# Performance work log

Measured on AMD Instinct MI355X. Metric: run time of the kernel, lower is better.

Reference implementation:

```python
import jax, jax.numpy as jnp
import numpy as np

INPUT_DIM, HIDDEN_DIM, N_HEADS, N_AGENTS = 256, 512, 8, 64
BATCH, N_ENTITIES = 128, 256


def setup_inputs() -> dict:
    key = jax.random.key(0)
    ks = jax.random.split(key, 6)
    x = jax.random.normal(ks[0], (BATCH, N_ENTITIES, INPUT_DIM), dtype=jnp.float32)
    # encode: LeakyReLU -> Linear(input_dim, hidden_dim)
    W_enc = jax.random.normal(ks[1], (INPUT_DIM, HIDDEN_DIM), dtype=jnp.float32) * (1.0 / np.sqrt(INPUT_DIM))
    b_enc = jnp.zeros((HIDDEN_DIM,), dtype=jnp.float32)
    # per-head full hidden x hidden projections, stacked on head axis
    WQ = jax.random.normal(ks[2], (N_HEADS, HIDDEN_DIM, HIDDEN_DIM), dtype=jnp.float32)
    WK = jax.random.normal(ks[3], (N_HEADS, HIDDEN_DIM, HIDDEN_DIM), dtype=jnp.float32)
    WV = jax.random.normal(ks[4], (N_HEADS, HIDDEN_DIM, HIDDEN_DIM), dtype=jnp.float32)
    return {"x": x, "W_enc": W_enc, "b_enc": b_enc, "WQ": WQ, "WK": WK, "WV": WV, "n_agents": N_AGENTS}


def reference(x, W_enc, b_enc, WQ, WK, WV, n_agents):
    scale = 1.0 / np.sqrt(WQ.shape[-1]).astype(np.float32)
    # encode: LeakyReLU(0.01) then Linear
    h = jax.nn.leaky_relu(x, negative_slope=0.01) @ W_enc + b_enc  # [b, e, H]
    ha = h[:, :n_agents]  # [b, a, H]
    # all heads at once: n = head axis
    Q = jnp.einsum('bah,nhd->nbad', ha, WQ)
    K = jnp.einsum('beh,nhd->nbed', h, WK)
    V = jnp.einsum('beh,nhd->nbed', h, WV)
    scores = jnp.einsum('nbad,nbed->nbae', Q, K) * scale
    p = jax.nn.softmax(scores, axis=-1)
    # redundant renormalization from the original code
    prob = p / (jnp.sum(p, axis=-1, keepdims=True) + 1e-12)
    z = jnp.einsum('nbae,nbed->nbad', prob, V)  # [n, b, a, H]
    return jnp.mean(z, axis=0)  # [b, a, H]
```

## Files before the change

kernel.cpp:

```cpp
#include <hip/hip_runtime.h>
#include <math.h>

#define BATCH  128
#define NENT   256
#define INDIM  256
#define HID    512
#define NHEAD  8
#define NAGENT 64
#define SCALE  0.04419417382415922f


typedef unsigned short u16;
typedef unsigned int   u32;

typedef __bf16 bf16x8  __attribute__((ext_vector_type(8)));
typedef float  floatx4 __attribute__((ext_vector_type(4)));
typedef u32    u32x4   __attribute__((ext_vector_type(4)));
typedef u32    u32x2   __attribute__((ext_vector_type(2)));

union Frag {
    u32x4 s;
    struct { u32x2 lo, hi; } p;
    bf16x8 v;
};

__device__ __forceinline__ u16 f2bf(float x) {
    u32 u = __float_as_uint(x);
    return (u16)((u + 0x7FFFu + ((u >> 16) & 1u)) >> 16);
}
__device__ __forceinline__ float bf2f(u16 b) {
    return __uint_as_float(((u32)b) << 16);
}
__device__ __forceinline__ void split4(const float4& r, ushort4& hh, ushort4& hl) {
    hh.x = f2bf(r.x); hl.x = f2bf(r.x - bf2f(hh.x));
    hh.y = f2bf(r.y); hl.y = f2bf(r.y - bf2f(hh.y));
    hh.z = f2bf(r.z); hl.z = f2bf(r.z - bf2f(hh.z));
    hh.w = f2bf(r.w); hl.w = f2bf(r.w - bf2f(hh.w));
}
__device__ __forceinline__ floatx4 mm(const Frag& a, const Frag& b, floatx4 c) {
    return __builtin_amdgcn_mfma_f32_16x16x32_bf16(a.v, b.v, c, 0, 0, 0);
}
__device__ __forceinline__ void gl16(const u16* g, char* l) {
    __builtin_amdgcn_global_load_lds(
        (const __attribute__((address_space(1))) u32*)g,
        (__attribute__((address_space(3))) u32*)l, 16, 0, 0);
}

__global__ __launch_bounds__(256) void wenc_t_kernel(const float* __restrict__ W,
                                                     u16* __restrict__ Wt_p) {
    __shared__ float tile[64][68];
    const int bid = blockIdx.x;
    const int k0 = (bid & 3) * 64;
    const int d0 = (bid >> 2) * 64;
    const int t = threadIdx.x;
    const int ki = t >> 2, dc = (t & 3) * 16;
    #pragma unroll
    for (int c = 0; c < 4; ++c)
        *(float4*)&tile[ki][dc + c * 4] =
            *(const float4*)(W + (size_t)(k0 + ki) * HID + d0 + dc + c * 4);
    __syncthreads();
    const int dr = t >> 2, kc = (t & 3) * 16;
    #pragma unroll
    for (int c = 0; c < 4; ++c) {
        float4 v = make_float4(tile[kc + c * 4 + 0][dr], tile[kc + c * 4 + 1][dr],
                               tile[kc + c * 4 + 2][dr], tile[kc + c * 4 + 3][dr]);
        ushort4 hh, hl; split4(v, hh, hl);
        const int kk = k0 + kc + c * 4;
        size_t o = (size_t)(d0 + dr) * 512 + (size_t)(kk >> 5) * 64 + (kk & 31);
        *(ushort4*)(Wt_p + o) = hh;
        *(ushort4*)(Wt_p + o + 32) = hl;
    }
}

__global__ __launch_bounds__(256) void enc_kernel(const float* __restrict__ x,
                                                  const u16* __restrict__ Wt_p,
                                                  const float* __restrict__ bias,
                                                  u16* __restrict__ h_p) {
    __shared__ u16 Ah[32][264];
    __shared__ u16 Al[32][264];
    const int r0 = blockIdx.x * 32;
    const int t  = threadIdx.x;
    {
        const int row = t >> 3;
        const float* xr = x + (size_t)(r0 + row) * INDIM;
        #pragma unroll
        for (int j = 0; j < 8; ++j) {
            const int k0 = ((t & 7) + j * 8) * 4;
            float4 v = *(const float4*)(xr + k0);
            v.x = v.x > 0.f ? v.x : 0.01f * v.x;
            v.y = v.y > 0.f ? v.y : 0.01f * v.y;
            v.z = v.z > 0.f ? v.z : 0.01f * v.z;
            v.w = v.w > 0.f ? v.w : 0.01f * v.w;
            ushort4 hh, hl; split4(v, hh, hl);
            *(ushort4*)&Ah[row][k0] = hh;
            *(ushort4*)&Al[row][k0] = hl;
        }
    }
    __syncthreads();

    const int wid = t >> 6, lane = t & 63, l15 = lane & 15, quad = lane >> 4;
    const int mbase = (wid & 1) * 16;
    const int nbase = (wid >> 1) * 256;
    const floatx4 z4 = {0.f, 0.f, 0.f, 0.f};
    floatx4 acc[16];
    #pragma unroll
    for (int i = 0; i < 16; ++i) acc[i] = z4;

    for (int ks = 0; ks < 8; ++ks) {
        const int k = ks * 32 + quad * 8;
        Frag Afh, Afl;
        Afh.s = *(const u32x4*)&Ah[mbase + l15][k];
        Afl.s = *(const u32x4*)&Al[mbase + l15][k];
        #pragma unroll
        for (int nt = 0; nt < 16; ++nt) {
            const int d = nbase + nt * 16 + l15;
            const size_t wo = (size_t)d * 512 + (size_t)ks * 64 + quad * 8;
            Frag Bh, Bl;
            Bh.s = *(const u32x4*)(Wt_p + wo);
            Bl.s = *(const u32x4*)(Wt_p + wo + 32);
            floatx4 c = acc[nt];
            c = __builtin_amdgcn_mfma_f32_16x16x32_bf16(Afh.v, Bh.v, c, 0, 0, 0);
            c = __builtin_amdgcn_mfma_f32_16x16x32_bf16(Afh.v, Bl.v, c, 0, 0, 0);
            c = __builtin_amdgcn_mfma_f32_16x16x32_bf16(Afl.v, Bh.v, c, 0, 0, 0);
            acc[nt] = c;
        }
    }
    #pragma unroll
    for (int nt = 0; nt < 16; ++nt) {
        const int d = nbase + nt * 16 + l15;
        const float bv = bias[d];
        #pragma unroll
        for (int r = 0; r < 4; ++r) {
            const float v = acc[nt][r] + bv;
            const u16 hi = f2bf(v);
            const u16 lo = f2bf(v - bf2f(hi));
            const size_t o = (size_t)(r0 + mbase + quad * 4 + r) * 1024
                           + (size_t)(d >> 5) * 64 + (d & 31);
            h_p[o]      = hi;
            h_p[o + 32] = lo;
        }
    }
}

__global__ __launch_bounds__(256) void ht_kernel(const u16* __restrict__ h_p,
                                                 u16* __restrict__ hT) {
    __shared__ u16 tile[64][72];
    const int bid = blockIdx.x;
    const int dt = bid & 7;
    const int et = (bid >> 3) & 3;
    const int b  = bid >> 5;
    const int t  = threadIdx.x;
    const int r  = t >> 2, cs = (t & 3) * 16;
    const int dg = dt * 64 + cs;
    const u16* src = h_p + (size_t)(b * 256 + et * 64 + r) * 1024
                   + (size_t)(dg >> 5) * 64 + (dg & 31);
    *(ushort4*)&tile[r][cs + 0]  = *(const ushort4*)(src + 0);
    *(ushort4*)&tile[r][cs + 4]  = *(const ushort4*)(src + 4);
    *(ushort4*)&tile[r][cs + 8]  = *(const ushort4*)(src + 8);
    *(ushort4*)&tile[r][cs + 12] = *(const ushort4*)(src + 12);
    __syncthreads();
    const int d = t >> 2, es = (t & 3) * 16;
    u16* dst = hT + (size_t)b * 131072 + (size_t)(dt * 64 + d) * 256 + et * 64 + es;
    #pragma unroll
    for (int c = 0; c < 4; ++c) {
        ushort4 v = make_ushort4(tile[es + c * 4 + 0][d], tile[es + c * 4 + 1][d],
                                 tile[es + c * 4 + 2][d], tile[es + c * 4 + 3][d]);
        *(ushort4*)(dst + c * 4) = v;
    }
}

__global__ __launch_bounds__(256) void wqk_kernel(const float* __restrict__ WQ,
                                                  const float* __restrict__ WK,
                                                  u16* __restrict__ Mt_p) {
    __shared__ u16 Ah[64][72], Al[64][72], Bh[64][72], Bl[64][72];
    const int bid = blockIdx.x;
    const int jt = (bid & 7) * 64;
    const int it = ((bid >> 3) & 7) * 64;
    const int n  = bid >> 6;
    const float* qp = WQ + (size_t)n * 262144;
    const float* kp = WK + (size_t)n * 262144;
    const int t = threadIdx.x;
    const int wid = t >> 6, lane = t & 63, l15 = lane & 15, quad = lane >> 4;
    const int srow = t >> 2, sc = (t & 3) * 16;

    const floatx4 z4 = {0.f, 0.f, 0.f, 0.f};
    floatx4 acc[4];
    #pragma unroll
    for (int i = 0; i < 4; ++i) acc[i] = z4;

    for (int kc = 0; kc < HID; kc += 64) {
        #pragma unroll
        for (int f = 0; f < 4; ++f) {
            float4 va = *(const float4*)(kp + (size_t)(jt + srow) * HID + kc + sc + f * 4);
            ushort4 hh, hl; split4(va, hh, hl);
            *(ushort4*)&Ah[srow][sc + f * 4] = hh;
            *(ushort4*)&Al[srow][sc + f * 4] = hl;
            float4 vb = *(const float4*)(qp + (size_t)(it + srow) * HID + kc + sc + f * 4);
            split4(vb, hh, hl);
            *(ushort4*)&Bh[srow][sc + f * 4] = hh;
            *(ushort4*)&Bl[srow][sc + f * 4] = hl;
        }
        __syncthreads();
        #pragma unroll
        for (int ks = 0; ks < 2; ++ks) {
            const int k = ks * 32 + quad * 8;
            Frag Afh, Afl;
            Afh.s = *(const u32x4*)&Ah[wid * 16 + l15][k];
            Afl.s = *(const u32x4*)&Al[wid * 16 + l15][k];
            #pragma unroll
            for (int nt = 0; nt < 4; ++nt) {
                Frag Bfh, Bfl;
                Bfh.s = *(const u32x4*)&Bh[nt * 16 + l15][k];
                Bfl.s = *(const u32x4*)&Bl[nt * 16 + l15][k];
                floatx4 c = acc[nt];
                c = __builtin_amdgcn_mfma_f32_16x16x32_bf16(Afh.v, Bfh.v, c, 0, 0, 0);
                c = __builtin_amdgcn_mfma_f32_16x16x32_bf16(Afh.v, Bfl.v, c, 0, 0, 0);
                c = __builtin_amdgcn_mfma_f32_16x16x32_bf16(Afl.v, Bfh.v, c, 0, 0, 0);
                acc[nt] = c;
            }
        }
        __syncthreads();
    }
    #pragma unroll
    for (int nt = 0; nt < 4; ++nt)
        #pragma unroll
        for (int r = 0; r < 4; ++r) {
            const float v = acc[nt][r] * SCALE;
            const u16 hi = f2bf(v);
            const u16 lo = f2bf(v - bf2f(hi));
            const int j = jt + wid * 16 + quad * 4 + r;
            const int i = it + nt * 16 + l15;
            const size_t o = (size_t)n * 524288 + (size_t)j * 1024
                           + (size_t)(i >> 5) * 64 + (i & 31);
            Mt_p[o]      = hi;
            Mt_p[o + 32] = lo;
        }
}

__global__ __launch_bounds__(256) void wvt_kernel(const float* __restrict__ WV,
                                                  u16* __restrict__ WVt) {
    __shared__ float tile[64][68];
    const int bid = blockIdx.x;
    const int i0 = (bid & 7) * 64;
    const int o0 = ((bid >> 3) & 7) * 64;
    const int n  = bid >> 6;
    const float* src = WV + (size_t)n * 262144;
    const int t  = threadIdx.x;
    const int di = t >> 2;
    const int dc = (t & 3) * 16;
    #pragma unroll
    for (int c = 0; c < 4; ++c)
        *(float4*)&tile[di][dc + c * 4] =
            *(const float4*)(src + (size_t)(i0 + di) * HID + o0 + dc + c * 4);
    __syncthreads();
    const int dr = t >> 2;
    const int ic = (t & 3) * 16;
    size_t o = (size_t)n * 262144 + (size_t)(o0 + dr) * HID + i0 + ic;
    #pragma unroll
    for (int c = 0; c < 4; ++c) {
        ushort4 v = make_ushort4(f2bf(tile[ic + c * 4 + 0][dr]), f2bf(tile[ic + c * 4 + 1][dr]),
                                 f2bf(tile[ic + c * 4 + 2][dr]), f2bf(tile[ic + c * 4 + 3][dr]));
        *(ushort4*)(WVt + o + c * 4) = v;
    }
}

template<bool USE_HT>
__global__ __launch_bounds__(256, 3) void attn_kernel(const u16* __restrict__ h_p,
                                                      const u16* __restrict__ Mt_p,
                                                      const u16* __restrict__ WVt,
                                                      const u16* __restrict__ hT,
                                                      float* __restrict__ out) {
    constexpr int SMSZ = USE_HT ? 37888 : 53504;
    __shared__ __align__(16) char SM[SMSZ];
    u16*   Th  = (u16*)SM;
    u16*   Tl  = (u16*)(SM + 16640);
    float* S   = (float*)SM;
    float* red = (float*)(SM + (USE_HT ? 36864 : 33792));
    u16*   HbT = (u16*)SM;
    u16*   U   = (u16*)SM;
    u16*   Pt  = (u16*)(SM + (USE_HT ? 0 : 36864));

    const int bid = blockIdx.x;
    const int x7 = bid & 7;
    const int s  = bid >> 3;
    const int at = s & 1;
    const int n  = (x7 >> 1) | (((s >> 1) & 1) << 2);
    const int b  = ((s >> 2) << 1) | (x7 & 1);

    const int tid  = threadIdx.x;
    const int wid  = tid >> 6;
    const int lane = tid & 63;
    const int l15  = lane & 15;
    const int quad = lane >> 4;

    const u16* Mtp = Mt_p + (size_t)n * 524288;
    const u16* Wv  = WVt  + (size_t)n * 262144;
    const u16* hTb = hT + (size_t)b * 131072;
    const size_t hb_base = (size_t)b * 262144;
    const size_t ha_row0 = hb_base + (size_t)(at * 32) * 1024;

    const floatx4 z4 = {0.f, 0.f, 0.f, 0.f};
    floatx4 Sacc[8];
    #pragma unroll
    for (int i = 0; i < 8; ++i) Sacc[i] = z4;

    for (int H = 0; H < 2; ++H) {
        __syncthreads();
        floatx4 Tacc[8];
        #pragma unroll
        for (int i = 0; i < 8; ++i) Tacc[i] = z4;
        const int d0 = H * 256;
        const u16* mtS = (const u16*)SM;
        const u16* haS = (const u16*)(SM + 32768);
        for (int ks = 0; ks < 16; ++ks) {
            #pragma unroll
            for (int j = 0; j < 8; ++j) {
                const int i = wid * 8 + j;
                const int chunk = i >> 2;
                const int row   = (i & 3) * 64 + lane;
                gl16(Mtp + (size_t)(d0 + row) * 1024 + ks * 64 + chunk * 8,
                     SM + i * 1024);
            }
            {
                const int chunk = wid * 2 + (lane >> 5);
                const int row   = lane & 31;
                gl16(h_p + ha_row0 + (size_t)row * 1024 + ks * 64 + chunk * 8,
                     SM + 32768 + wid * 1024);
            }
            __syncthreads();
            Frag Ah0, Al0, Ah1, Al1;
            Ah0.s = *(const u32x4*)(haS + ((quad)     * 32 + l15)      * 8);
            Al0.s = *(const u32x4*)(haS + ((4 + quad) * 32 + l15)      * 8);
            Ah1.s = *(const u32x4*)(haS + ((quad)     * 32 + 16 + l15) * 8);
            Al1.s = *(const u32x4*)(haS + ((4 + quad) * 32 + 16 + l15) * 8);
            #pragma unroll
            for (int nt = 0; nt < 4; ++nt) {
                const int row = (wid * 4 + nt) * 16 + l15;
                Frag Bh, Bl;
                Bh.s = *(const u32x4*)(mtS + ((quad)     * 256 + row) * 8);
                Bl.s = *(const u32x4*)(mtS + ((4 + quad) * 256 + row) * 8);
                floatx4 c0 = Tacc[nt], c1 = Tacc[4 + nt];
                c0 = mm(Ah0, Bh, c0); c0 = mm(Ah0, Bl, c0); c0 = mm(Al0, Bh, c0);
                c1 = mm(Ah1, Bh, c1); c1 = mm(Ah1, Bl, c1); c1 = mm(Al1, Bh, c1);
                Tacc[nt] = c0; Tacc[4 + nt] = c1;
            }
            __syncthreads();
        }
        #pragma unroll
        for (int mt = 0; mt < 2; ++mt)
            #pragma unroll
            for (int nt = 0; nt < 4; ++nt)
                #pragma unroll
                for (int r = 0; r < 4; ++r) {
                    const float v = Tacc[mt * 4 + nt][r];
                    const int a  = mt * 16 + quad * 4 + r;
                    const int dl = (wid * 4 + nt) * 16 + l15;
                    const u16 hi = f2bf(v);
                    Th[a * 260 + dl] = hi;
                    Tl[a * 260 + dl] = f2bf(v - bf2f(hi));
                }
        __syncthreads();
        for (int ks = 0; ks < 8; ++ks) {
            const int kl = ks * 32 + quad * 8;
            const int ko = (H * 8 + ks) * 64 + quad * 8;
            Frag Ahf[4], Alf[4];
            #pragma unroll
            for (int mt = 0; mt < 4; ++mt) {
                const size_t ro = hb_base + (size_t)((wid * 4 + mt) * 16 + l15) * 1024 + ko;
                Ahf[mt].s = *(const u32x4*)(h_p + ro);
                Alf[mt].s = *(const u32x4*)(h_p + ro + 32);
            }
            #pragma unroll
            for (int nt = 0; nt < 2; ++nt) {
                const int ac = nt * 16 + l15;
                Frag Bfh, Bfl;
                Bfh.p.lo = *(const u32x2*)(Th + ac * 260 + kl);
                Bfh.p.hi = *(const u32x2*)(Th + ac * 260 + kl + 4);
                Bfl.p.lo = *(const u32x2*)(Tl + ac * 260 + kl);
                Bfl.p.hi = *(const u32x2*)(Tl + ac * 260 + kl + 4);
                #pragma unroll
                for (int mt = 0; mt < 4; ++mt) {
                    floatx4 c = Sacc[mt * 2 + nt];
                    c = __builtin_amdgcn_mfma_f32_16x16x32_bf16(Ahf[mt].v, Bfh.v, c, 0, 0, 0);
                    c = __builtin_amdgcn_mfma_f32_16x16x32_bf16(Ahf[mt].v, Bfl.v, c, 0, 0, 0);
                    c = __builtin_amdgcn_mfma_f32_16x16x32_bf16(Alf[mt].v, Bfh.v, c, 0, 0, 0);
                    Sacc[mt * 2 + nt] = c;
                }
            }
        }
    }
    __syncthreads();
    #pragma unroll
    for (int mt = 0; mt < 4; ++mt)
        #pragma unroll
        for (int nt = 0; nt < 2; ++nt)
            #pragma unroll
            for (int r = 0; r < 4; ++r) {
                const int e = (wid * 4 + mt) * 16 + quad * 4 + r;
                const int a = nt * 16 + l15;
                S[e * 33 + a] = Sacc[mt * 2 + nt][r];
            }
    __syncthreads();
    {
        const int a   = tid & 31;
        const int seg = tid >> 5;
        float v[32];
        #pragma unroll
        for (int i = 0; i < 32; ++i) v[i] = S[(seg * 32 + i) * 33 + a];
        float mx = v[0];
        #pragma unroll
        for (int i = 1; i < 32; ++i) mx = fmaxf(mx, v[i]);
        red[a * 8 + seg] = mx;
        __syncthreads();
        float gmx = red[a * 8 + 0];
        #pragma unroll
        for (int i = 1; i < 8; ++i) gmx = fmaxf(gmx, red[a * 8 + i]);
        __syncthreads();
        float sum = 0.f;
        #pragma unroll
        for (int i = 0; i < 32; ++i) { v[i] = expf(v[i] - gmx); sum += v[i]; }
        red[a * 8 + seg] = sum;
        __syncthreads();
        float tot = 0.f;
        #pragma unroll
        for (int i = 0; i < 8; ++i) tot += red[a * 8 + i];
        const float inv = 1.0f / tot;
        #pragma unroll
        for (int i = 0; i < 32; ++i)
            Pt[a * 260 + seg * 32 + i] = f2bf(v[i] * inv);
    }
    __syncthreads();
    floatx4 Uacc[16];
    #pragma unroll
    for (int i = 0; i < 16; ++i) Uacc[i] = z4;
    const int d0w = wid * 128;
    if (USE_HT) {
        for (int ep = 0; ep < 4; ++ep) {
            Frag Bc[2][8];
            #pragma unroll
            for (int sb = 0; sb < 2; ++sb)
                #pragma unroll
                for (int dt = 0; dt < 8; ++dt) {
                    const int d = d0w + dt * 16 + l15;
                    Bc[sb][dt].s = *(const u32x4*)(hTb + (size_t)d * 256
                                                   + (2 * ep + sb) * 32 + quad * 8);
                }
            #pragma unroll
            for (int sb = 0; sb < 2; ++sb) {
                const int et = 2 * ep + sb;
                Frag Ap[2];
                #pragma unroll
                for (int mt = 0; mt < 2; ++mt) {
                    const int ar = mt * 16 + l15;
                    Ap[mt].p.lo = *(const u32x2*)(Pt + ar * 260 + et * 32 + quad * 8);
                    Ap[mt].p.hi = *(const u32x2*)(Pt + ar * 260 + et * 32 + quad * 8 + 4);
                }
                #pragma unroll
                for (int dt = 0; dt < 8; ++dt)
                    #pragma unroll
                    for (int mt = 0; mt < 2; ++mt)
                        Uacc[mt * 8 + dt] = __builtin_amdgcn_mfma_f32_16x16x32_bf16(
                            Ap[mt].v, Bc[sb][dt].v, Uacc[mt * 8 + dt], 0, 0, 0);
            }
        }
    } else {
        u32* Hb32 = (u32*)HbT;
        for (int et = 0; et < 8; ++et) {
            {
                const int epi = lane & 15;
                const int q   = lane >> 4;
                const size_t r0p = hb_base + (size_t)(et * 32 + 2 * epi) * 1024;
                #pragma unroll
                for (int c = 0; c < 4; ++c) {
                    const int d0c = d0w + c * 32 + q * 8;
                    const size_t po = (size_t)(d0c >> 5) * 64 + (d0c & 31);
                    u32x4 u0 = *(const u32x4*)(h_p + r0p + po);
                    u32x4 u1 = *(const u32x4*)(h_p + r0p + 1024 + po);
                    #pragma unroll
                    for (int p = 0; p < 4; ++p) {
                        const u32 w0 = (u0[p] & 0xFFFFu) | (u1[p] << 16);
                        const u32 w1 = (u0[p] >> 16) | (u1[p] & 0xFFFF0000u);
                        Hb32[(d0c + 2 * p) * 18 + epi]     = w0;
                        Hb32[(d0c + 2 * p + 1) * 18 + epi] = w1;
                    }
                }
            }
            Frag Ap[2];
            #pragma unroll
            for (int mt = 0; mt < 2; ++mt) {
                const int ar = mt * 16 + l15;
                Ap[mt].p.lo = *(const u32x2*)(Pt + ar * 260 + et * 32 + quad * 8);
                Ap[mt].p.hi = *(const u32x2*)(Pt + ar * 260 + et * 32 + quad * 8 + 4);
            }
            #pragma unroll
            for (int dt = 0; dt < 8; ++dt) {
                const int d = d0w + dt * 16 + l15;
                Frag Bf;
                Bf.p.lo = *(const u32x2*)(HbT + d * 36 + quad * 8);
                Bf.p.hi = *(const u32x2*)(HbT + d * 36 + quad * 8 + 4);
                #pragma unroll
                for (int mt = 0; mt < 2; ++mt)
                    Uacc[mt * 8 + dt] = __builtin_amdgcn_mfma_f32_16x16x32_bf16(
                        Ap[mt].v, Bf.v, Uacc[mt * 8 + dt], 0, 0, 0);
            }
        }
    }
    __syncthreads();
    #pragma unroll
    for (int mt = 0; mt < 2; ++mt)
        #pragma unroll
        for (int dt = 0; dt < 8; ++dt)
            #pragma unroll
            for (int r = 0; r < 4; ++r) {
                const int a = mt * 16 + quad * 4 + r;
                const int d = d0w + dt * 16 + l15;
                U[a * 520 + d] = f2bf(Uacc[mt * 8 + dt][r]);
            }
    __syncthreads();
    floatx4 Zacc[16];
    #pragma unroll
    for (int i = 0; i < 16; ++i) Zacc[i] = z4;
    for (int kp = 0; kp < 8; ++kp) {
        Frag Bw[2][8];
        #pragma unroll
        for (int sb = 0; sb < 2; ++sb) {
            const int k = (kp * 2 + sb) * 32 + quad * 8;
            #pragma unroll
            for (int dt = 0; dt < 8; ++dt) {
                const int dn = (wid * 8 + dt) * 16 + l15;
                Bw[sb][dt].s = *(const u32x4*)(Wv + (size_t)dn * HID + k);
            }
        }
        #pragma unroll
        for (int sb = 0; sb < 2; ++sb) {
            const int k = (kp * 2 + sb) * 32 + quad * 8;
            Frag Au[2];
            #pragma unroll
            for (int mt = 0; mt < 2; ++mt) {
                Au[mt].p.lo = *(const u32x2*)(U + (mt * 16 + l15) * 520 + k);
                Au[mt].p.hi = *(const u32x2*)(U + (mt * 16 + l15) * 520 + k + 4);
            }
            #pragma unroll
            for (int dt = 0; dt < 8; ++dt)
                #pragma unroll
                for (int mt = 0; mt < 2; ++mt)
                    Zacc[mt * 8 + dt] = __builtin_amdgcn_mfma_f32_16x16x32_bf16(
                        Au[mt].v, Bw[sb][dt].v, Zacc[mt * 8 + dt], 0, 0, 0);
        }
    }
    float* ob = out + ((size_t)b * NAGENT + at * 32) * HID;
    #pragma unroll
    for (int mt = 0; mt < 2; ++mt)
        #pragma unroll
        for (int dt = 0; dt < 8; ++dt)
            #pragma unroll
            for (int r = 0; r < 4; ++r) {
                const int a  = mt * 16 + quad * 4 + r;
                const int dn = (wid * 8 + dt) * 16 + l15;
                atomicAdd(ob + (size_t)a * HID + dn, Zacc[mt * 8 + dt][r] * 0.125f);
            }
}

extern "C" void kernel_launch(void* const* d_in, const int* in_sizes, int n_in,
                              void* d_out, int out_size, void* d_ws, size_t ws_size,
                              hipStream_t stream) {
    const float* x     = (const float*)d_in[0];
    const float* W_enc = (const float*)d_in[1];
    const float* b_enc = (const float*)d_in[2];
    const float* WQ    = (const float*)d_in[3];
    const float* WK    = (const float*)d_in[4];
    const float* WV    = (const float*)d_in[5];
    float* out = (float*)d_out;

    char* ws = (char*)d_ws;
    u16* h_p  = (u16*)ws;
    u16* Mt_p = (u16*)(ws + 67108864);
    u16* WVt  = (u16*)(ws + 75497472);
    u16* hT   = (u16*)(ws + 79691776);
    u16* Wt_p = WVt;

    const bool useHT = ws_size >= (size_t)113246208;

    hipMemsetAsync(d_out, 0, (size_t)out_size * sizeof(float), stream);
    wenc_t_kernel<<<32, 256, 0, stream>>>(W_enc, Wt_p);
    enc_kernel<<<1024, 256, 0, stream>>>(x, Wt_p, b_enc, h_p);
    if (useHT) ht_kernel<<<4096, 256, 0, stream>>>(h_p, hT);
    wvt_kernel<<<512, 256, 0, stream>>>(WV, WVt);
    wqk_kernel<<<512, 256, 0, stream>>>(WQ, WK, Mt_p);
    if (useHT)
        attn_kernel<true><<<2048, 256, 0, stream>>>(h_p, Mt_p, WVt, hT, out);
    else
        attn_kernel<false><<<2048, 256, 0, stream>>>(h_p, Mt_p, WVt, hT, out);
}
```

Measured before the change: 894.5 us.

## Stage MFMA B-operands through LDS with direct global-to-LDS loads

Three GEMM phases of the attention kernel now load their global operands with a gl16 global-to-shared primitive into an LDS staging buffer, then read the MFMA fragments from LDS. Before, each lane issued strided 16-byte global loads straight into registers. The goal is coalesced loads and lower register pressure. The cost is extra __syncthreads barriers per k-step, more LDS (USE_HT grows to 51200 bytes), no double buffering, and a remapped output column index in the final projection.

```diff
diff --git a/kernel.cpp b/kernel.cpp
--- a/kernel.cpp
+++ b/kernel.cpp
@@ -270,12 +270,12 @@
                                                       const u16* __restrict__ WVt,
                                                       const u16* __restrict__ hT,
                                                       float* __restrict__ out) {
-    constexpr int SMSZ = USE_HT ? 37888 : 53504;
+    constexpr int SMSZ = USE_HT ? 51200 : 53504;
     __shared__ __align__(16) char SM[SMSZ];
     u16*   Th  = (u16*)SM;
     u16*   Tl  = (u16*)(SM + 16640);
     float* S   = (float*)SM;
-    float* red = (float*)(SM + (USE_HT ? 36864 : 33792));
+    float* red = (float*)(SM + (USE_HT ? 50176 : 33792));
     u16*   HbT = (u16*)SM;
     u16*   U   = (u16*)SM;
     u16*   Pt  = (u16*)(SM + (USE_HT ? 0 : 36864));
@@ -360,32 +360,69 @@
                     Tl[a * 260 + dl] = f2bf(v - bf2f(hi));
                 }
         __syncthreads();
-        for (int ks = 0; ks < 8; ++ks) {
-            const int kl = ks * 32 + quad * 8;
-            const int ko = (H * 8 + ks) * 64 + quad * 8;
-            Frag Ahf[4], Alf[4];
-            #pragma unroll
-            for (int mt = 0; mt < 4; ++mt) {
-                const size_t ro = hb_base + (size_t)((wid * 4 + mt) * 16 + l15) * 1024 + ko;
-                Ahf[mt].s = *(const u32x4*)(h_p + ro);
-                Alf[mt].s = *(const u32x4*)(h_p + ro + 32);
-            }
-            #pragma unroll
-            for (int nt = 0; nt < 2; ++nt) {
-                const int ac = nt * 16 + l15;
-                Frag Bfh, Bfl;
-                Bfh.p.lo = *(const u32x2*)(Th + ac * 260 + kl);
-                Bfh.p.hi = *(const u32x2*)(Th + ac * 260 + kl + 4);
-                Bfl.p.lo = *(const u32x2*)(Tl + ac * 260 + kl);
-                Bfl.p.hi = *(const u32x2*)(Tl + ac * 260 + kl + 4);
+        {
+            const u16* Bs = (const u16*)(SM + 33792);
+            for (int ks = 0; ks < 8; ++ks) {
+                const int ko = (H * 8 + ks) * 64;
+                const int kl = ks * 32 + quad * 8;
                 #pragma unroll
-                for (int mt = 0; mt < 4; ++mt) {
-                    floatx4 c = Sacc[mt * 2 + nt];
-                    c = __builtin_amdgcn_mfma_f32_16x16x32_bf16(Ahf[mt].v, Bfh.v, c, 0, 0, 0);
-                    c = __builtin_amdgcn_mfma_f32_16x16x32_bf16(Ahf[mt].v, Bfl.v, c, 0, 0, 0);
-                    c = __builtin_amdgcn_mfma_f32_16x16x32_bf16(Alf[mt].v, Bfh.v, c, 0, 0, 0);
-                    Sacc[mt * 2 + nt] = c;
+                for (int j = 0; j < 4; ++j) {
+                    const int i = wid * 4 + j;
+                    gl16(h_p + hb_base + (size_t)((i & 3) * 64 + lane) * 1024
+                             + ko + (i >> 2) * 8,
+                         SM + 33792 + i * 1024);
                 }
+                __syncthreads();
+                {
+                    Frag Ahf[4];
+                    #pragma unroll
+                    for (int mt = 0; mt < 4; ++mt)
+                        Ahf[mt].s = *(const u32x4*)(Bs
+                            + ((size_t)quad * 256 + (wid * 4 + mt) * 16 + l15) * 8);
+                    #pragma unroll
+                    for (int nt = 0; nt < 2; ++nt) {
+                        const int ac = nt * 16 + l15;
+                        Frag Bfh, Bfl;
+                        Bfh.p.lo = *(const u32x2*)(Th + ac * 260 + kl);
+                        Bfh.p.hi = *(const u32x2*)(Th + ac * 260 + kl + 4);
+                        Bfl.p.lo = *(const u32x2*)(Tl + ac * 260 + kl);
+                        Bfl.p.hi = *(const u32x2*)(Tl + ac * 260 + kl + 4);
+                        #pragma unroll
+                        for (int mt = 0; mt < 4; ++mt) {
+                            floatx4 c = Sacc[mt * 2 + nt];
+                            c = mm(Ahf[mt], Bfh, c);
+                            c = mm(Ahf[mt], Bfl, c);
+                            Sacc[mt * 2 + nt] = c;
+                        }
+                    }
+                }
+                __syncthreads();
+                #pragma unroll
+                for (int j = 0; j < 4; ++j) {
+                    const int i = wid * 4 + j;
+                    gl16(h_p + hb_base + (size_t)((i & 3) * 64 + lane) * 1024
+                             + ko + 32 + (i >> 2) * 8,
+                         SM + 33792 + i * 1024);
+                }
+                __syncthreads();
+                {
+                    Frag Alf[4];
+                    #pragma unroll
+                    for (int mt = 0; mt < 4; ++mt)
+                        Alf[mt].s = *(const u32x4*)(Bs
+                            + ((size_t)quad * 256 + (wid * 4 + mt) * 16 + l15) * 8);
+                    #pragma unroll
+                    for (int nt = 0; nt < 2; ++nt) {
+                        const int ac = nt * 16 + l15;
+                        Frag Bfh;
+                        Bfh.p.lo = *(const u32x2*)(Th + ac * 260 + kl);
+                        Bfh.p.hi = *(const u32x2*)(Th + ac * 260 + kl + 4);
+                        #pragma unroll
+                        for (int mt = 0; mt < 4; ++mt)
+                            Sacc[mt * 2 + nt] = mm(Alf[mt], Bfh, Sacc[mt * 2 + nt]);
+                    }
+                }
+                __syncthreads();
             }
         }
     }
@@ -435,33 +472,31 @@
     for (int i = 0; i < 16; ++i) Uacc[i] = z4;
     const int d0w = wid * 128;
     if (USE_HT) {
-        for (int ep = 0; ep < 4; ++ep) {
-            Frag Bc[2][8];
-            #pragma unroll
-            for (int sb = 0; sb < 2; ++sb)
+        const u16* Cs = (const u16*)(SM + 16640);
+        for (int et = 0; et < 8; ++et) {
+            #pragma unroll
+            for (int j = 0; j < 8; ++j) {
+                const int i = wid * 8 + j;
+                gl16(hTb + (size_t)((i & 7) * 64 + lane) * 256 + et * 32 + (i >> 3) * 8,
+                     SM + 16640 + i * 1024);
+            }
+            __syncthreads();
+            Frag Ap[2];
+            #pragma unroll
+            for (int mt = 0; mt < 2; ++mt) {
+                const int ar = mt * 16 + l15;
+                Ap[mt].p.lo = *(const u32x2*)(Pt + ar * 260 + et * 32 + quad * 8);
+                Ap[mt].p.hi = *(const u32x2*)(Pt + ar * 260 + et * 32 + quad * 8 + 4);
+            }
+            #pragma unroll
+            for (int dt = 0; dt < 8; ++dt) {
+                Frag Bf;
+                Bf.s = *(const u32x4*)(Cs + ((size_t)quad * 512 + d0w + dt * 16 + l15) * 8);
                 #pragma unroll
-                for (int dt = 0; dt < 8; ++dt) {
-                    const int d = d0w + dt * 16 + l15;
-                    Bc[sb][dt].s = *(const u32x4*)(hTb + (size_t)d * 256
-                                                   + (2 * ep + sb) * 32 + quad * 8);
-                }
-            #pragma unroll
-            for (int sb = 0; sb < 2; ++sb) {
-                const int et = 2 * ep + sb;
-                Frag Ap[2];
-                #pragma unroll
-                for (int mt = 0; mt < 2; ++mt) {
-                    const int ar = mt * 16 + l15;
-                    Ap[mt].p.lo = *(const u32x2*)(Pt + ar * 260 + et * 32 + quad * 8);
-                    Ap[mt].p.hi = *(const u32x2*)(Pt + ar * 260 + et * 32 + quad * 8 + 4);
-                }
-                #pragma unroll
-                for (int dt = 0; dt < 8; ++dt)
-                    #pragma unroll
-                    for (int mt = 0; mt < 2; ++mt)
-                        Uacc[mt * 8 + dt] = __builtin_amdgcn_mfma_f32_16x16x32_bf16(
-                            Ap[mt].v, Bc[sb][dt].v, Uacc[mt * 8 + dt], 0, 0, 0);
-            }
+                for (int mt = 0; mt < 2; ++mt)
+                    Uacc[mt * 8 + dt] = mm(Ap[mt], Bf, Uacc[mt * 8 + dt]);
+            }
+            __syncthreads();
         }
     } else {
         u32* Hb32 = (u32*)HbT;
@@ -520,33 +555,40 @@
     floatx4 Zacc[16];
     #pragma unroll
     for (int i = 0; i < 16; ++i) Zacc[i] = z4;
-    for (int kp = 0; kp < 8; ++kp) {
-        Frag Bw[2][8];
-        #pragma unroll
-        for (int sb = 0; sb < 2; ++sb) {
-            const int k = (kp * 2 + sb) * 32 + quad * 8;
-            #pragma unroll
-            for (int dt = 0; dt < 8; ++dt) {
-                const int dn = (wid * 8 + dt) * 16 + l15;
-                Bw[sb][dt].s = *(const u32x4*)(Wv + (size_t)dn * HID + k);
-            }
-        }
-        #pragma unroll
-        for (int sb = 0; sb < 2; ++sb) {
-            const int k = (kp * 2 + sb) * 32 + quad * 8;
-            Frag Au[2];
-            #pragma unroll
-            for (int mt = 0; mt < 2; ++mt) {
-                Au[mt].p.lo = *(const u32x2*)(U + (mt * 16 + l15) * 520 + k);
-                Au[mt].p.hi = *(const u32x2*)(U + (mt * 16 + l15) * 520 + k + 4);
-            }
-            #pragma unroll
-            for (int dt = 0; dt < 8; ++dt)
+    {
+        const u16* Ds = (const u16*)(SM + 33792);
+        for (int kp = 0; kp < 8; ++kp)
+            #pragma unroll
+            for (int sb = 0; sb < 2; ++sb)
                 #pragma unroll
-                for (int mt = 0; mt < 2; ++mt)
-                    Zacc[mt * 8 + dt] = __builtin_amdgcn_mfma_f32_16x16x32_bf16(
-                        Au[mt].v, Bw[sb][dt].v, Zacc[mt * 8 + dt], 0, 0, 0);
-        }
+                for (int h = 0; h < 2; ++h) {
+                    #pragma unroll
+                    for (int j = 0; j < 4; ++j) {
+                        const int i = wid * 4 + j;
+                        gl16(Wv + (size_t)(h * 256 + (i & 3) * 64 + lane) * 512
+                                 + (kp * 2 + sb) * 32 + (i >> 2) * 8,
+                             SM + 33792 + i * 1024);
+                    }
+                    __syncthreads();
+                    const int k = (kp * 2 + sb) * 32 + quad * 8;
+                    Frag Au[2];
+                    #pragma unroll
+                    for (int mt = 0; mt < 2; ++mt) {
+                        Au[mt].p.lo = *(const u32x2*)(U + (mt * 16 + l15) * 520 + k);
+                        Au[mt].p.hi = *(const u32x2*)(U + (mt * 16 + l15) * 520 + k + 4);
+                    }
+                    #pragma unroll
+                    for (int t2 = 0; t2 < 4; ++t2) {
+                        Frag Bw;
+                        Bw.s = *(const u32x4*)(Ds
+                            + ((size_t)quad * 256 + (t2 * 4 + wid) * 16 + l15) * 8);
+                        const int dt = h * 4 + t2;
+                        #pragma unroll
+                        for (int mt = 0; mt < 2; ++mt)
+                            Zacc[mt * 8 + dt] = mm(Au[mt], Bw, Zacc[mt * 8 + dt]);
+                    }
+                    __syncthreads();
+                }
     }
     float* ob = out + ((size_t)b * NAGENT + at * 32) * HID;
     #pragma unroll
@@ -556,7 +598,7 @@
             #pragma unroll
             for (int r = 0; r < 4; ++r) {
                 const int a  = mt * 16 + quad * 4 + r;
-                const int dn = (wid * 8 + dt) * 16 + l15;
+                const int dn = (dt * 4 + wid) * 16 + l15;
                 atomicAdd(ob + (size_t)a * HID + dn, Zacc[mt * 8 + dt][r] * 0.125f);
             }
 }
```

Result: slower. 970.2 us (+8.5%).

## Double-buffer Mt and h_a staging in the Q·K^T projection loop

Applied to the files above, without the earlier changes.

Splits the per-k-step Mt tile load into two halves with separate LDS buffers and double-buffers the h_a tile. The next half is issued with async global-to-LDS copies while MFMAs run on the current half, overlapping loads with compute instead of a serial load-sync-compute-sync sequence. LDS use rises for the USE_HT variant, which may reduce occupancy, and the number of barriers per k-step stays the same. The interleaved half-tile index mapping is more complex and must stay consistent with the consumer reads.

```diff
diff --git a/kernel.cpp b/kernel.cpp
--- a/kernel.cpp
+++ b/kernel.cpp
@@ -270,12 +270,12 @@
                                                       const u16* __restrict__ WVt,
                                                       const u16* __restrict__ hT,
                                                       float* __restrict__ out) {
-    constexpr int SMSZ = USE_HT ? 37888 : 53504;
+    constexpr int SMSZ = USE_HT ? 41984 : 53504;
     __shared__ __align__(16) char SM[SMSZ];
     u16*   Th  = (u16*)SM;
     u16*   Tl  = (u16*)(SM + 16640);
     float* S   = (float*)SM;
-    float* red = (float*)(SM + (USE_HT ? 36864 : 33792));
+    float* red = (float*)(SM + (USE_HT ? 40960 : 33792));
     u16*   HbT = (u16*)SM;
     u16*   U   = (u16*)SM;
     u16*   Pt  = (u16*)(SM + (USE_HT ? 0 : 36864));
@@ -304,47 +304,60 @@
     #pragma unroll
     for (int i = 0; i < 8; ++i) Sacc[i] = z4;
 
+#define STAGE_MT(KS, HH, BUF) do {                                                   \
+        _Pragma("unroll")                                                            \
+        for (int j = 0; j < 4; ++j) {                                                \
+            const int i  = wid * 4 + j;                                              \
+            const int ch = i >> 1;                                                   \
+            const int rh = (i & 1) * 64 + lane;                                      \
+            const int rw = (rh >> 5) * 64 + (HH) * 32 + (rh & 31);                   \
+            gl16(Mtp + (size_t)(d0 + rw) * 1024 + (KS) * 64 + ch * 8,                \
+                 SM + (BUF) * 16384 + i * 1024);                                     \
+        } } while (0)
+#define STAGE_HA(KS, BUF) do {                                                       \
+        gl16(h_p + ha_row0 + (size_t)(lane & 31) * 1024 + (KS) * 64                  \
+                 + (wid * 2 + (lane >> 5)) * 8,                                      \
+             SM + 32768 + (BUF) * 4096 + wid * 1024); } while (0)
+
     for (int H = 0; H < 2; ++H) {
         __syncthreads();
         floatx4 Tacc[8];
         #pragma unroll
         for (int i = 0; i < 8; ++i) Tacc[i] = z4;
         const int d0 = H * 256;
-        const u16* mtS = (const u16*)SM;
-        const u16* haS = (const u16*)(SM + 32768);
+        STAGE_MT(0, 0, 0);
+        STAGE_HA(0, 0);
+        __syncthreads();
         for (int ks = 0; ks < 16; ++ks) {
-            #pragma unroll
-            for (int j = 0; j < 8; ++j) {
-                const int i = wid * 8 + j;
-                const int chunk = i >> 2;
-                const int row   = (i & 3) * 64 + lane;
-                gl16(Mtp + (size_t)(d0 + row) * 1024 + ks * 64 + chunk * 8,
-                     SM + i * 1024);
-            }
-            {
-                const int chunk = wid * 2 + (lane >> 5);
-                const int row   = lane & 31;
-                gl16(h_p + ha_row0 + (size_t)row * 1024 + ks * 64 + chunk * 8,
-                     SM + 32768 + wid * 1024);
-            }
-            __syncthreads();
-            Frag Ah0, Al0, Ah1, Al1;
-            Ah0.s = *(const u32x4*)(haS + ((quad)     * 32 + l15)      * 8);
-            Al0.s = *(const u32x4*)(haS + ((4 + quad) * 32 + l15)      * 8);
-            Ah1.s = *(const u32x4*)(haS + ((quad)     * 32 + 16 + l15) * 8);
-            Al1.s = *(const u32x4*)(haS + ((4 + quad) * 32 + 16 + l15) * 8);
-            #pragma unroll
-            for (int nt = 0; nt < 4; ++nt) {
-                const int row = (wid * 4 + nt) * 16 + l15;
-                Frag Bh, Bl;
-                Bh.s = *(const u32x4*)(mtS + ((quad)     * 256 + row) * 8);
-                Bl.s = *(const u32x4*)(mtS + ((4 + quad) * 256 + row) * 8);
-                floatx4 c0 = Tacc[nt], c1 = Tacc[4 + nt];
-                c0 = mm(Ah0, Bh, c0); c0 = mm(Ah0, Bl, c0); c0 = mm(Al0, Bh, c0);
-                c1 = mm(Ah1, Bh, c1); c1 = mm(Ah1, Bl, c1); c1 = mm(Al1, Bh, c1);
-                Tacc[nt] = c0; Tacc[4 + nt] = c1;
-            }
-            __syncthreads();
+            const u16* haS = (const u16*)(SM + 32768 + (ks & 1) * 4096);
+            #pragma unroll
+            for (int h = 0; h < 2; ++h) {
+                if (h == 0) {
+                    STAGE_MT(ks, 1, 1);
+                    STAGE_HA((ks + 1) & 15, (ks + 1) & 1);
+                } else if (ks < 15) {
+                    STAGE_MT(ks + 1, 0, 0);
+                }
+                const u16* mtS = (const u16*)(SM + h * 16384);
+                Frag Ah0, Al0, Ah1, Al1;
+                Ah0.s = *(const u32x4*)(haS + ((quad)     * 32 + l15) * 8);
+                Al0.s = *(const u32x4*)(haS + ((4 + quad) * 32 + l15) * 8);
+                Ah1.s = *(const u32x4*)(haS + ((quad)     * 32 + 16 + l15) * 8);
+                Al1.s = *(const u32x4*)(haS + ((4 + quad) * 32 + 16 + l15) * 8);
+                #pragma unroll
+                for (int ntl = 0; ntl < 2; ++ntl) {
+                    const int rh = wid * 32 + ntl * 16 + l15;
+                    Frag Bh, Bl;
+                    Bh.s = *(const u32x4*)(mtS + ((quad)     * 128 + rh) * 8);
+                    Bl.s = *(const u32x4*)(mtS + ((4 + quad) * 128 + rh) * 8);
+                    const int nt = h * 2 + ntl;
+                    floatx4 c0 = Tacc[nt], c1 = Tacc[4 + nt];
+                    c0 = mm(Ah0, Bh, c0); c0 = mm(Ah0, Bl, c0); c0 = mm(Al0, Bh, c0);
+                    c1 = mm(Ah1, Bh, c1); c1 = mm(Ah1, Bl, c1); c1 = mm(Al1, Bh, c1);
+                    Tacc[nt] = c0; Tacc[4 + nt] = c1;
+                }
+                __syncthreads();
+            }
         }
         #pragma unroll
         for (int mt = 0; mt < 2; ++mt)
@@ -559,6 +572,8 @@
                 const int dn = (wid * 8 + dt) * 16 + l15;
                 atomicAdd(ob + (size_t)a * HID + dn, Zacc[mt * 8 + dt][r] * 0.125f);
             }
+#undef STAGE_MT
+#undef STAGE_HA
 }
 
 extern "C" void kernel_launch(void* const* d_in, const int* in_sizes, int n_in,
```

After: 892.7 us. About the same (-0.2%).
